# Kernel optimization log

Measured on AMD Instinct MI355X. Metric: run time of the kernel, lower is better.

The kernel has to match this reference:

```python
import jax, jax.numpy as jnp
import numpy as np


def setup_inputs() -> dict:
    key = jax.random.key(0)
    ks = jax.random.split(key, 5)
    B, N, D = 32, 128, 4096
    return {
        "curr_head": jax.random.normal(ks[0], (B, D), jnp.float32),
        "curr_errors": jax.random.normal(ks[1], (B, N, D), jnp.float32),
        "curr_head_2": jax.random.normal(ks[2], (B, D), jnp.float32),
        "curr_errors_2": jax.random.normal(ks[3], (B, N, D), jnp.float32),
        "adv_errors": jax.random.normal(ks[4], (B, N, D), jnp.float32),
        "shared_errors": 128,
    }


def reference(curr_head, curr_errors, curr_head_2, curr_errors_2, adv_errors, shared_errors):
    B = curr_head.shape[0]
    tail = curr_head.shape[1:]
    # (B, N, *tail) -> (N, B, *tail), matching torch's view + transpose(1, 0)
    e1 = jnp.moveaxis(curr_errors.reshape(B, -1, *tail), 1, 0)
    e2 = jnp.moveaxis(curr_errors_2.reshape(B, -1, *tail), 1, 0)
    N1, N2 = e1.shape[0], e2.shape[0]
    s = int(shared_errors)

    def zeros(n):
        return jnp.zeros((n, B) + tail, e1.dtype)

    # self_errors / factor_errors: (N1 + N2 - s, B, *tail)
    self_errors = jnp.concatenate([e1, zeros(N2 - s)], axis=0)
    factor_errors = jnp.concatenate([e2[:s], zeros(N1 - s), e2[s:]], axis=0)

    lin_err = curr_head[None] * factor_errors + curr_head_2[None] * self_errors
    quadr_const = self_errors * factor_errors

    # Exact identity: 0.5*sum_ij |a_i a_j + a_j a_i| = (sum_i |a_i|)^2 (elementwise),
    # since a_i*a_j is already symmetric. Avoids the (N,N,B,*tail) outer product.
    abs_sum = jnp.abs(self_errors).sum(axis=0)
    quadr_error = abs_sum * abs_sum - 0.5 * jnp.abs(quadr_const).sum(axis=0)

    new_head = curr_head * curr_head_2 + 0.5 * quadr_const.sum(axis=0)

    errors = jnp.moveaxis(lin_err, 0, 1)  # (B, N1+N2-s, *tail)
    new_errors = jnp.concatenate([errors, quadr_error[:, None] * adv_errors], axis=1)
    new_errors = new_errors.reshape(-1, *tail)
    return new_head, new_errors
```

## Files before the change

kernel.cpp:

```cpp
#include <hip/hip_runtime.h>

constexpr int B  = 32;
constexpr int N  = 128;
constexpr int D  = 4096;
constexpr int DV = D / 4;

constexpr int COLS  = 64;
constexpr int TILES = DV / COLS;
constexpr int CH    = 4;
constexpr int TPB   = COLS * CH;
constexpr int ROWS  = 32;
constexpr int RG    = N / ROWS;
constexpr int NPC   = ROWS / CH;
constexpr int BATCH = 4;
constexpr int NBT   = NPC / BATCH;

constexpr long WS_F4 = (long)3 * RG * B * DV;

typedef float f4 __attribute__((ext_vector_type(4)));

__device__ __forceinline__ f4 f4abs(f4 a) {
    f4 r;
    r.x = fabsf(a.x); r.y = fabsf(a.y); r.z = fabsf(a.z); r.w = fabsf(a.w);
    return r;
}

__global__ __launch_bounds__(TPB) void k1_lin_partials(
    const float* __restrict__ h1,
    const float* __restrict__ e1,
    const float* __restrict__ h2,
    const float* __restrict__ e2,
    float* __restrict__ out,
    float* __restrict__ ws)
{
    const int lane  = threadIdx.x & (COLS - 1);
    const int chunk = threadIdx.x / COLS;
    const int bid   = blockIdx.x;
    const int tile  = bid % TILES;
    const int rowg  = (bid / TILES) % RG;
    const int b     = bid / (TILES * RG);
    const long d0   = ((long)tile * COLS + lane) * 4;

    const f4* e1p = (const f4*)(e1 + (long)b * N * D + d0);
    const f4* e2p = (const f4*)(e2 + (long)b * N * D + d0);
    f4* lin_out   = (f4*)(out + (long)B * D + (long)b * (2 * N) * D + d0);

    const f4 vh1 = *(const f4*)(h1 + (long)b * D + d0);
    const f4 vh2 = *(const f4*)(h2 + (long)b * D + d0);

    f4 sq  = (f4)(0.f);
    f4 sa  = (f4)(0.f);
    f4 saq = (f4)(0.f);

    const int n0 = rowg * ROWS + chunk * NPC;

    f4 Aa[2][BATCH], Ff[2][BATCH];
#pragma unroll
    for (int j = 0; j < BATCH; ++j) {
        const long off = (long)(n0 + j) * DV;
        Aa[0][j] = e1p[off];
        Ff[0][j] = e2p[off];
    }
#pragma unroll
    for (int bt = 0; bt < NBT; ++bt) {
        const int cur = bt & 1, nxt = cur ^ 1;
        if (bt < NBT - 1) {
#pragma unroll
            for (int j = 0; j < BATCH; ++j) {
                const long off = (long)(n0 + (bt + 1) * BATCH + j) * DV;
                Aa[nxt][j] = e1p[off];
                Ff[nxt][j] = e2p[off];
            }
        }
#pragma unroll
        for (int j = 0; j < BATCH; ++j) {
            const long off = (long)(n0 + bt * BATCH + j) * DV;
            f4 a = Aa[cur][j];
            f4 f = Ff[cur][j];
            lin_out[off] = vh1 * f + vh2 * a;
            f4 q = a * f;
            sq  += q;
            sa  += f4abs(a);
            saq += f4abs(q);
        }
    }

    __shared__ f4 s_q [CH][COLS];
    __shared__ f4 s_a [CH][COLS];
    __shared__ f4 s_aq[CH][COLS];
    s_q [chunk][lane] = sq;
    s_a [chunk][lane] = sa;
    s_aq[chunk][lane] = saq;
    __syncthreads();

    if (chunk == 0) {
        f4 tq  = s_q [0][lane];
        f4 ta  = s_a [0][lane];
        f4 taq = s_aq[0][lane];
#pragma unroll
        for (int c = 1; c < CH; ++c) {
            tq  += s_q [c][lane];
            ta  += s_a [c][lane];
            taq += s_aq[c][lane];
        }
        f4* ws4 = (f4*)ws;
        const long col = (long)tile * COLS + lane;
        ws4[(((long)0 * RG + rowg) * B + b) * DV + col] = tq;
        ws4[(((long)1 * RG + rowg) * B + b) * DV + col] = ta;
        ws4[(((long)2 * RG + rowg) * B + b) * DV + col] = taq;
    }
}

__global__ __launch_bounds__(TPB) void k2_adv_scale(
    const float* __restrict__ h1,
    const float* __restrict__ h2,
    const float* __restrict__ adv,
    float* __restrict__ out,
    const float* __restrict__ ws)
{
    const int lane  = threadIdx.x & (COLS - 1);
    const int chunk = threadIdx.x / COLS;
    const int bid   = blockIdx.x;
    const int tile  = bid % TILES;
    const int rowg  = (bid / TILES) % RG;
    const int b     = bid / (TILES * RG);
    const long d0   = ((long)tile * COLS + lane) * 4;
    const long col  = (long)tile * COLS + lane;

    const f4* advp = (const f4*)(adv + (long)b * N * D + d0);
    f4* adv_out    = (f4*)(out + (long)B * D + (long)b * (2 * N) * D
                               + (long)N * D + d0);

    const int n0 = rowg * ROWS + chunk * NPC;

    f4 V[NPC];
#pragma unroll
    for (int j = 0; j < NPC; ++j)
        V[j] = advp[(long)(n0 + j) * DV];

    const f4* ws4 = (const f4*)ws;
    f4 tq  = (f4)(0.f);
    f4 ta  = (f4)(0.f);
    f4 taq = (f4)(0.f);
#pragma unroll
    for (int r = 0; r < RG; ++r) {
        tq  += ws4[(((long)0 * RG + r) * B + b) * DV + col];
        ta  += ws4[(((long)1 * RG + r) * B + b) * DV + col];
        taq += ws4[(((long)2 * RG + r) * B + b) * DV + col];
    }
    const f4 qe = ta * ta - 0.5f * taq;

    if (rowg == 0 && chunk == 0) {
        const f4 vh1 = *(const f4*)(h1 + (long)b * D + d0);
        const f4 vh2 = *(const f4*)(h2 + (long)b * D + d0);
        *(f4*)(out + (long)b * D + d0) = vh1 * vh2 + 0.5f * tq;
    }

#pragma unroll
    for (int j = 0; j < NPC; ++j)
        adv_out[(long)(n0 + j) * DV] = qe * V[j];
}

extern "C" void kernel_launch(void* const* d_in, const int* in_sizes, int n_in,
                              void* d_out, int out_size, void* d_ws, size_t ws_size,
                              hipStream_t stream) {
    const float* h1  = (const float*)d_in[0];
    const float* e1  = (const float*)d_in[1];
    const float* h2  = (const float*)d_in[2];
    const float* e2  = (const float*)d_in[3];
    const float* adv = (const float*)d_in[4];
    float* out = (float*)d_out;
    float* ws  = (float*)d_ws;

    dim3 grid(B * TILES * RG);
    dim3 block(TPB);
    k1_lin_partials<<<grid, block, 0, stream>>>(h1, e1, h2, e2, out, ws);
    k2_adv_scale  <<<grid, block, 0, stream>>>(h1, h2, adv, out, ws);
}
```

Before: 290.0 us.

## Widen column tiles, drop shared-memory reduction, and pipeline adv loads in k2

Each block now covers 256 float4 columns with one thread per column, walking 16 rows (8 row groups) in place of four 64-column chunks reduced through shared memory. This removes the LDS reduction and the __syncthreads, and every thread writes its own workspace partials. k2 now double-buffers the adv loads in batches and reads the tq partials only in row group 0. The trade-off is twice as many workspace partials for k2 to sum, and fewer blocks with more rows per thread.

```diff
diff --git a/kernel.cpp b/kernel.cpp
--- a/kernel.cpp
+++ b/kernel.cpp
@@ -5,17 +5,14 @@
 constexpr int D  = 4096;
 constexpr int DV = D / 4;
 
-constexpr int COLS  = 64;
-constexpr int TILES = DV / COLS;
-constexpr int CH    = 4;
-constexpr int TPB   = COLS * CH;
-constexpr int ROWS  = 32;
-constexpr int RG    = N / ROWS;
-constexpr int NPC   = ROWS / CH;
-constexpr int BATCH = 4;
-constexpr int NBT   = NPC / BATCH;
-
-constexpr long WS_F4 = (long)3 * RG * B * DV;
+constexpr int TPB     = 256;
+constexpr int TILE_F4 = TPB;
+constexpr int TILES   = DV / TILE_F4;
+constexpr int RG      = 8;
+constexpr int ROWS    = N / RG;
+constexpr int BATCH   = 4;
+constexpr int NBT     = ROWS / BATCH;
+constexpr int GRID    = B * TILES * RG;
 
 typedef float f4 __attribute__((ext_vector_type(4)));
 
@@ -33,26 +30,25 @@
     float* __restrict__ out,
     float* __restrict__ ws)
 {
-    const int lane  = threadIdx.x & (COLS - 1);
-    const int chunk = threadIdx.x / COLS;
-    const int bid   = blockIdx.x;
-    const int tile  = bid % TILES;
-    const int rowg  = (bid / TILES) % RG;
-    const int b     = bid / (TILES * RG);
-    const long d0   = ((long)tile * COLS + lane) * 4;
+    const int tid  = threadIdx.x;
+    const int bid  = blockIdx.x;
+    const int tile = bid % TILES;
+    const int rowg = (bid / TILES) % RG;
+    const int b    = bid / (TILES * RG);
+    const long col = (long)tile * TILE_F4 + tid;
 
-    const f4* e1p = (const f4*)(e1 + (long)b * N * D + d0);
-    const f4* e2p = (const f4*)(e2 + (long)b * N * D + d0);
-    f4* lin_out   = (f4*)(out + (long)B * D + (long)b * (2 * N) * D + d0);
+    const f4* e1p = (const f4*)(e1 + (long)b * N * D) + col;
+    const f4* e2p = (const f4*)(e2 + (long)b * N * D) + col;
+    f4* lin_out   = (f4*)(out + (long)B * D + (long)b * (2 * N) * D) + col;
 
-    const f4 vh1 = *(const f4*)(h1 + (long)b * D + d0);
-    const f4 vh2 = *(const f4*)(h2 + (long)b * D + d0);
+    const f4 vh1 = ((const f4*)(h1 + (long)b * D))[col];
+    const f4 vh2 = ((const f4*)(h2 + (long)b * D))[col];
 
-    f4 sq  = (f4)(0.f);
-    f4 sa  = (f4)(0.f);
-    f4 saq = (f4)(0.f);
+    f4 tq  = (f4)(0.f);
+    f4 ta  = (f4)(0.f);
+    f4 taq = (f4)(0.f);
 
-    const int n0 = rowg * ROWS + chunk * NPC;
+    const int n0 = rowg * ROWS;
 
     f4 Aa[2][BATCH], Ff[2][BATCH];
 #pragma unroll
@@ -79,36 +75,16 @@
             f4 f = Ff[cur][j];
             lin_out[off] = vh1 * f + vh2 * a;
             f4 q = a * f;
-            sq  += q;
-            sa  += f4abs(a);
-            saq += f4abs(q);
+            tq  += q;
+            ta  += f4abs(a);
+            taq += f4abs(q);
         }
     }
 
-    __shared__ f4 s_q [CH][COLS];
-    __shared__ f4 s_a [CH][COLS];
-    __shared__ f4 s_aq[CH][COLS];
-    s_q [chunk][lane] = sq;
-    s_a [chunk][lane] = sa;
-    s_aq[chunk][lane] = saq;
-    __syncthreads();
-
-    if (chunk == 0) {
-        f4 tq  = s_q [0][lane];
-        f4 ta  = s_a [0][lane];
-        f4 taq = s_aq[0][lane];
-#pragma unroll
-        for (int c = 1; c < CH; ++c) {
-            tq  += s_q [c][lane];
-            ta  += s_a [c][lane];
-            taq += s_aq[c][lane];
-        }
-        f4* ws4 = (f4*)ws;
-        const long col = (long)tile * COLS + lane;
-        ws4[(((long)0 * RG + rowg) * B + b) * DV + col] = tq;
-        ws4[(((long)1 * RG + rowg) * B + b) * DV + col] = ta;
-        ws4[(((long)2 * RG + rowg) * B + b) * DV + col] = taq;
-    }
+    f4* ws4 = (f4*)ws;
+    ws4[(((long)0 * RG + rowg) * B + b) * DV + col] = tq;
+    ws4[(((long)1 * RG + rowg) * B + b) * DV + col] = ta;
+    ws4[(((long)2 * RG + rowg) * B + b) * DV + col] = taq;
 }
 
 __global__ __launch_bounds__(TPB) void k2_adv_scale(
@@ -118,47 +94,56 @@
     float* __restrict__ out,
     const float* __restrict__ ws)
 {
-    const int lane  = threadIdx.x & (COLS - 1);
-    const int chunk = threadIdx.x / COLS;
-    const int bid   = blockIdx.x;
-    const int tile  = bid % TILES;
-    const int rowg  = (bid / TILES) % RG;
-    const int b     = bid / (TILES * RG);
-    const long d0   = ((long)tile * COLS + lane) * 4;
-    const long col  = (long)tile * COLS + lane;
+    const int tid  = threadIdx.x;
+    const int bid  = blockIdx.x;
+    const int tile = bid % TILES;
+    const int rowg = (bid / TILES) % RG;
+    const int b    = bid / (TILES * RG);
+    const long col = (long)tile * TILE_F4 + tid;
 
-    const f4* advp = (const f4*)(adv + (long)b * N * D + d0);
+    const f4* advp = (const f4*)(adv + (long)b * N * D) + col;
     f4* adv_out    = (f4*)(out + (long)B * D + (long)b * (2 * N) * D
-                               + (long)N * D + d0);
+                               + (long)N * D) + col;
 
-    const int n0 = rowg * ROWS + chunk * NPC;
+    const int n0 = rowg * ROWS;
 
-    f4 V[NPC];
+    f4 Vv[2][BATCH];
 #pragma unroll
-    for (int j = 0; j < NPC; ++j)
-        V[j] = advp[(long)(n0 + j) * DV];
+    for (int j = 0; j < BATCH; ++j)
+        Vv[0][j] = advp[(long)(n0 + j) * DV];
 
     const f4* ws4 = (const f4*)ws;
-    f4 tq  = (f4)(0.f);
     f4 ta  = (f4)(0.f);
     f4 taq = (f4)(0.f);
 #pragma unroll
     for (int r = 0; r < RG; ++r) {
-        tq  += ws4[(((long)0 * RG + r) * B + b) * DV + col];
         ta  += ws4[(((long)1 * RG + r) * B + b) * DV + col];
         taq += ws4[(((long)2 * RG + r) * B + b) * DV + col];
     }
     const f4 qe = ta * ta - 0.5f * taq;
 
-    if (rowg == 0 && chunk == 0) {
-        const f4 vh1 = *(const f4*)(h1 + (long)b * D + d0);
-        const f4 vh2 = *(const f4*)(h2 + (long)b * D + d0);
-        *(f4*)(out + (long)b * D + d0) = vh1 * vh2 + 0.5f * tq;
+    if (rowg == 0) {
+        f4 tq = (f4)(0.f);
+#pragma unroll
+        for (int r = 0; r < RG; ++r)
+            tq += ws4[(((long)0 * RG + r) * B + b) * DV + col];
+        const f4 vh1 = ((const f4*)(h1 + (long)b * D))[col];
+        const f4 vh2 = ((const f4*)(h2 + (long)b * D))[col];
+        ((f4*)out)[(long)b * DV + col] = vh1 * vh2 + 0.5f * tq;
     }
 
 #pragma unroll
-    for (int j = 0; j < NPC; ++j)
-        adv_out[(long)(n0 + j) * DV] = qe * V[j];
+    for (int bt = 0; bt < NBT; ++bt) {
+        const int cur = bt & 1, nxt = cur ^ 1;
+        if (bt < NBT - 1) {
+#pragma unroll
+            for (int j = 0; j < BATCH; ++j)
+                Vv[nxt][j] = advp[(long)(n0 + (bt + 1) * BATCH + j) * DV];
+        }
+#pragma unroll
+        for (int j = 0; j < BATCH; ++j)
+            adv_out[(long)(n0 + bt * BATCH + j) * DV] = qe * Vv[cur][j];
+    }
 }
 
 extern "C" void kernel_launch(void* const* d_in, const int* in_sizes, int n_in,
@@ -172,7 +157,7 @@
     float* out = (float*)d_out;
     float* ws  = (float*)d_ws;
 
-    dim3 grid(B * TILES * RG);
+    dim3 grid(GRID);
     dim3 block(TPB);
     k1_lin_partials<<<grid, block, 0, stream>>>(h1, e1, h2, e2, out, ws);
     k2_adv_scale  <<<grid, block, 0, stream>>>(h1, h2, adv, out, ws);
```

New measurement: 294.6 us. Within noise of the previous version (+1.6%).
